# Kernel tuning notes

Hardware: AMD Instinct MI355X
Metric: run time of the kernel (lower is better)

## Reference

```python
import jax, jax.numpy as jnp
import numpy as np

BLOCK = 64       # _aether_cfg['block_size']
JL_DIM = 32      # epsilon_jl_bridge d_out
EPS_GOV = 0.5    # fixed governor eps (governor.target)
ROPE_BASE = 10000.0
RMS_EPS = 1e-6


def _normalize(x, axis=-1):
    n = jnp.sqrt(jnp.sum(x * x, axis=axis, keepdims=True))
    return x / jnp.maximum(n, 1e-12)


def _rms_norm(x):
    return x * jax.lax.rsqrt(jnp.mean(x * x, axis=-1, keepdims=True) + RMS_EPS)


def _rope(x, cos, sin):
    half = x.shape[-1] // 2
    x1, x2 = x[..., :half], x[..., half:]
    return jnp.concatenate([x1 * cos + x2 * sin, -x1 * sin + x2 * cos], axis=-1)


def setup_inputs() -> dict:
    key = jax.random.key(0)
    ks = jax.random.split(key, 6)
    B, S, Dm, H = 2, 2048, 2048, 16
    sc = 1.0 / np.sqrt(Dm)
    x = jax.random.normal(ks[0], (B, S, Dm), jnp.float32)
    Wq = jax.random.normal(ks[1], (Dm, Dm), jnp.float32) * sc
    Wk = jax.random.normal(ks[2], (Dm, Dm), jnp.float32) * sc
    Wv = jax.random.normal(ks[3], (Dm, Dm), jnp.float32) * sc
    Wo = jax.random.normal(ks[4], (Dm, Dm), jnp.float32) * sc
    q_gain = jnp.ones((H,), jnp.float32)
    return {"x": x, "Wq": Wq, "Wk": Wk, "Wv": Wv, "Wo": Wo, "q_gain": q_gain}


def reference(x, Wq, Wk, Wv, Wo, q_gain):
    B, S, Dm = x.shape
    H = q_gain.shape[0]
    Dh = Dm // H

    # QKV projections (bias-free linear, torch weight layout [out,in])
    q = (x @ Wq.T).reshape(B, S, H, Dh).transpose(0, 2, 1, 3)  # (B,H,S,Dh)
    k = (x @ Wk.T).reshape(B, S, H, Dh).transpose(0, 2, 1, 3)
    v = (x @ Wv.T).reshape(B, S, H, Dh).transpose(0, 2, 1, 3)

    # RoPE tables
    inv_freq = 1.0 / (ROPE_BASE ** (jnp.arange(0, Dh, 2, dtype=jnp.float32) / Dh))
    freqs = jnp.outer(jnp.arange(S, dtype=jnp.float32), inv_freq)  # (S,Dh/2)
    cos = jnp.cos(freqs)[None, None]
    sin = jnp.sin(freqs)[None, None]

    q = _rope(_rms_norm(q), cos, sin) * q_gain[None, :, None, None]
    k = _rope(_rms_norm(k), cos, sin)

    # --- aether sparse SDPA: JL block bounds -> top-k blocks -> gather -> SDPA ---
    N = S // BLOCK  # number of KV blocks (static)
    proj = jax.random.normal(jax.random.key(42), (Dh, JL_DIM), jnp.float32) / np.sqrt(JL_DIM)

    q_proj = _normalize(q.mean(axis=2, keepdims=True) @ proj)          # (B,H,1,JL)
    k_blocks = k.reshape(B, H, N, BLOCK, Dh)
    k_proj = _normalize(k_blocks @ proj)                               # (B,H,N,BLOCK,JL)
    centroids = _normalize(k_proj.mean(axis=3))                        # (B,H,N,JL)
    radii = jnp.clip(
        1.0 - jnp.min(jnp.sum(k_proj * centroids[:, :, :, None, :], axis=-1), axis=-1),
        0.0, 1.0)                                                      # (B,H,N)
    ub = jnp.einsum('bhqj,bhnj->bhqn', q_proj, centroids) + radii[:, :, None, :]
    scores = ub[:, :, 0, :]                                            # (B,H,N)
    # force-include the last two blocks (union in the original code)
    scores = scores.at[:, :, N - 2:].set(jnp.inf)

    n_keep = max(2, int(N * min(1.0, EPS_GOV))) + 2                    # static
    _, top_idx = jax.lax.top_k(scores, n_keep)                         # (B,H,n_keep)
    top_idx = jnp.sort(top_idx, axis=-1)
    idx = (top_idx[..., None] * BLOCK + jnp.arange(BLOCK)).reshape(B, H, -1)  # (B,H,K)

    k_s = jnp.take_along_axis(k, idx[..., None], axis=2)               # (B,H,K,Dh)
    v_s = jnp.take_along_axis(v, idx[..., None], axis=2)

    att = jax.nn.softmax(
        jnp.einsum('bhqd,bhkd->bhqk', q, k_s) / np.sqrt(Dh), axis=-1)  # (B,H,S,K)
    y = jnp.einsum('bhqk,bhkd->bhqd', att, v_s)                        # (B,H,S,Dh)

    y = y.transpose(0, 2, 1, 3).reshape(B, S, Dm)
    return y @ Wo.T
```

## Files before the change

### kernel.cpp

```cpp
#include <hip/hip_runtime.h>
#include <hip/hip_bf16.h>

#define B_ 2
#define S_ 2048
#define DM 2048
#define H_ 16
#define DH 128
#define NBLK 32
#define NKEEP 18
#define BH (B_ * H_)

typedef __attribute__((ext_vector_type(8))) short short8;
typedef __attribute__((ext_vector_type(8))) _Float16 f16x8;
typedef __attribute__((ext_vector_type(4))) _Float16 f16x4;
typedef __attribute__((ext_vector_type(4))) float f32x4;

#define GLOAD16(gp, lp)                                                        \
  __builtin_amdgcn_global_load_lds(                                            \
      (const __attribute__((address_space(1))) unsigned int*)(const void*)(gp),\
      (__attribute__((address_space(3))) unsigned int*)(void*)(lp), 16, 0, 0)

__device__ __forceinline__ unsigned short f32_to_bf16(float f) {
  unsigned u = __float_as_uint(f);
  unsigned r = (u + 0x7fffu + ((u >> 16) & 1u)) >> 16;
  return (unsigned short)r;
}
__device__ __forceinline__ float bf16_to_f32(unsigned short h) {
  return __uint_as_float(((unsigned)h) << 16);
}
__device__ __forceinline__ float fexp2(float x) {
  float r;
  asm("v_exp_f32 %0, %1" : "=v"(r) : "v"(x));
  return r;
}

__device__ __forceinline__ unsigned rotl32(unsigned x, int r) {
  return (x << r) | (x >> (32 - r));
}

__device__ __forceinline__ float erfinv_f32(float x) {
  float w = -log1pf(-x * x);
  float p;
  if (w < 5.0f) {
    w -= 2.5f;
    p = 2.81022636e-08f;
    p = fmaf(p, w, 3.43273939e-07f);
    p = fmaf(p, w, -3.5233877e-06f);
    p = fmaf(p, w, -4.39150654e-06f);
    p = fmaf(p, w, 0.00021858087f);
    p = fmaf(p, w, -0.00125372503f);
    p = fmaf(p, w, -0.00417768164f);
    p = fmaf(p, w, 0.246640727f);
    p = fmaf(p, w, 1.50140941f);
  } else {
    w = sqrtf(w) - 3.0f;
    p = -0.000200214257f;
    p = fmaf(p, w, 0.000100950558f);
    p = fmaf(p, w, 0.00134934322f);
    p = fmaf(p, w, -0.00367342844f);
    p = fmaf(p, w, 0.00573950773f);
    p = fmaf(p, w, -0.0076224613f);
    p = fmaf(p, w, 0.00943887047f);
    p = fmaf(p, w, 1.00167406f);
    p = fmaf(p, w, 2.83297682f);
  }
  return p * x;
}

__device__ __forceinline__ float bits_to_normal(unsigned b) {
  float f = __uint_as_float((b >> 9) | 0x3f800000u) - 1.0f;
  const float lo = -0.9999999403953552f;
  float u = fmaxf(lo, fmaf(f, 2.0f, lo));
  return 1.4142135623730951f * erfinv_f32(u);
}

__global__ void tables_kernel(float* __restrict__ proj,
                              float* __restrict__ cosb,
                              float* __restrict__ sinb) {
  if (blockIdx.x < 16) {
    int i = blockIdx.x * 256 + threadIdx.x;
    unsigned k0 = 0u, k1 = 42u;
    unsigned k2 = 0x1BD11BDAu ^ k0 ^ k1;
    unsigned x0 = 0u, x1 = (unsigned)i;
    x0 += k0; x1 += k1;
#define QR(r) { x0 += x1; x1 = rotl32(x1, r); x1 ^= x0; }
    QR(13) QR(15) QR(26) QR(6)   x0 += k1; x1 += k2 + 1u;
    QR(17) QR(29) QR(16) QR(24)  x0 += k2; x1 += k0 + 2u;
    QR(13) QR(15) QR(26) QR(6)   x0 += k0; x1 += k1 + 3u;
    QR(17) QR(29) QR(16) QR(24)  x0 += k1; x1 += k2 + 4u;
    QR(13) QR(15) QR(26) QR(6)   x0 += k2; x1 += k0 + 5u;
#undef QR
    proj[i] = bits_to_normal(x0 ^ x1) / 5.656854249492381f;
  } else {
    int s = blockIdx.x - 16;
    int j = threadIdx.x;
    if (j < 64) {
      double e = (double)(2 * j) / 128.0;
      double invf = 1.0 / pow(10000.0, e);
      float freq = (float)s * (float)invf;
      cosb[s * 64 + j] = (float)cos((double)freq);
      sinb[s * 64 + j] = (float)sin((double)freq);
    }
  }
}

__global__ __launch_bounds__(256) void split_x3_kernel(const float* __restrict__ in,
                                                       unsigned short* __restrict__ hi,
                                                       unsigned short* __restrict__ lo,
                                                       _Float16* __restrict__ f16,
                                                       int n4) {
  int i = blockIdx.x * blockDim.x + threadIdx.x;
  if (i >= n4) return;
  float4 v = ((const float4*)in)[i];
  ushort4 hv, lv;
  f16x4 fv;
  hv.x = f32_to_bf16(v.x); lv.x = f32_to_bf16(v.x - bf16_to_f32(hv.x)); fv[0] = (_Float16)v.x;
  hv.y = f32_to_bf16(v.y); lv.y = f32_to_bf16(v.y - bf16_to_f32(hv.y)); fv[1] = (_Float16)v.y;
  hv.z = f32_to_bf16(v.z); lv.z = f32_to_bf16(v.z - bf16_to_f32(hv.z)); fv[2] = (_Float16)v.z;
  hv.w = f32_to_bf16(v.w); lv.w = f32_to_bf16(v.w - bf16_to_f32(hv.w)); fv[3] = (_Float16)v.w;
  ((ushort4*)hi)[i] = hv;
  ((ushort4*)lo)[i] = lv;
  ((f16x4*)f16)[i] = fv;
}

__global__ __launch_bounds__(256) void split_w3_kernel(const float* __restrict__ wk,
                                                       const float* __restrict__ wq,
                                                       const float* __restrict__ wv,
                                                       unsigned short* __restrict__ khi,
                                                       unsigned short* __restrict__ klo,
                                                       _Float16* __restrict__ qf,
                                                       _Float16* __restrict__ vf,
                                                       int n4) {
  int i = blockIdx.x * blockDim.x + threadIdx.x;
  if (i >= n4) return;
  {
    float4 v = ((const float4*)wk)[i];
    ushort4 hv, lv;
    hv.x = f32_to_bf16(v.x); lv.x = f32_to_bf16(v.x - bf16_to_f32(hv.x));
    hv.y = f32_to_bf16(v.y); lv.y = f32_to_bf16(v.y - bf16_to_f32(hv.y));
    hv.z = f32_to_bf16(v.z); lv.z = f32_to_bf16(v.z - bf16_to_f32(hv.z));
    hv.w = f32_to_bf16(v.w); lv.w = f32_to_bf16(v.w - bf16_to_f32(hv.w));
    ((ushort4*)khi)[i] = hv;
    ((ushort4*)klo)[i] = lv;
  }
  {
    float4 v = ((const float4*)wq)[i];
    f16x4 fv;
    fv[0] = (_Float16)v.x; fv[1] = (_Float16)v.y;
    fv[2] = (_Float16)v.z; fv[3] = (_Float16)v.w;
    ((f16x4*)qf)[i] = fv;
  }
  {
    float4 v = ((const float4*)wv)[i];
    f16x4 fv;
    fv[0] = (_Float16)v.x; fv[1] = (_Float16)v.y;
    fv[2] = (_Float16)v.z; fv[3] = (_Float16)v.w;
    ((f16x4*)vf)[i] = fv;
  }
}

__global__ __launch_bounds__(256) void split_f16_kernel(const float* __restrict__ in,
                                                        _Float16* __restrict__ f16,
                                                        int n4) {
  int i = blockIdx.x * blockDim.x + threadIdx.x;
  if (i >= n4) return;
  float4 v = ((const float4*)in)[i];
  f16x4 fv;
  fv[0] = (_Float16)v.x; fv[1] = (_Float16)v.y;
  fv[2] = (_Float16)v.z; fv[3] = (_Float16)v.w;
  ((f16x4*)f16)[i] = fv;
}

__global__ __launch_bounds__(512, 2) void mfma_gemm_k_sk(const unsigned short* __restrict__ Ahi,
                                                         const unsigned short* __restrict__ Alo,
                                                         const unsigned short* __restrict__ Whi,
                                                         const unsigned short* __restrict__ Wlo,
                                                         float* __restrict__ kp0,
                                                         float* __restrict__ kp1) {
  __shared__ char smem[131072];
  const int t = threadIdx.x, l = t & 63, w = t >> 6;
  const int lin = blockIdx.z * 128 + blockIdx.y * 8 + blockIdx.x;
  const int swz = (lin & 7) * 32 + (lin >> 3);
  const int kz = swz >> 7;
  const int idx = swz & 127;
  const int n0 = (idx & 7) * 256;
  const int m0 = (idx >> 3) * 256;
  const int kbase = kz * 1024;
  float* C = kz ? kp1 : kp0;
  const int wm = w >> 2, wn = w & 3;
  const int lr = l & 15;
  const int lg8 = (l >> 4) * 8;
  const size_t rstep = (size_t)16 * DM;

  const unsigned short* gAh = Ahi + (size_t)(m0 + w * 32 + lr) * DM + lg8;
  const unsigned short* gAl = Alo + (size_t)(m0 + w * 32 + lr) * DM + lg8;
  const unsigned short* gBh = Whi + (size_t)(n0 + w * 32 + lr) * DM + lg8;
  const unsigned short* gBl = Wlo + (size_t)(n0 + w * 32 + lr) * DM + lg8;

  f32x4 acc[8][4];
#pragma unroll
  for (int i = 0; i < 8; ++i)
#pragma unroll
    for (int j = 0; j < 4; ++j) acc[i][j] = (f32x4){0.f, 0.f, 0.f, 0.f};

  {
    char* base = smem + w * 2048;
    GLOAD16(gAh + kbase, base);
    GLOAD16(gAh + rstep + kbase, base + 1024);
    GLOAD16(gAl + kbase, base + 16384);
    GLOAD16(gAl + rstep + kbase, base + 16384 + 1024);
    GLOAD16(gBh + kbase, base + 32768);
    GLOAD16(gBh + rstep + kbase, base + 32768 + 1024);
    GLOAD16(gBl + kbase, base + 49152);
    GLOAD16(gBl + rstep + kbase, base + 49152 + 1024);
  }
  int cur = 0;

#define KQUAD(q)                                                                        \
  {                                                                                     \
    short8 ah0 = *(const short8*)(buf + (wm * 8 + 2 * (q)) * 1024 + l * 16);            \
    short8 ah1 = *(const short8*)(buf + (wm * 8 + 2 * (q) + 1) * 1024 + l * 16);        \
    short8 al0 = *(const short8*)(buf + 16384 + (wm * 8 + 2 * (q)) * 1024 + l * 16);    \
    short8 al1 = *(const short8*)(buf + 16384 + (wm * 8 + 2 * (q) + 1) * 1024 + l * 16);\
    __builtin_amdgcn_s_setprio(1);                                                      \
    _Pragma("unroll")                                                                   \
    for (int n = 0; n < 4; ++n) {                                                       \
      acc[2 * (q)][n] = __builtin_amdgcn_mfma_f32_16x16x32_bf16(ah0, bh[n], acc[2 * (q)][n], 0, 0, 0); \
      acc[2 * (q)][n] = __builtin_amdgcn_mfma_f32_16x16x32_bf16(ah0, bl[n], acc[2 * (q)][n], 0, 0, 0); \
      acc[2 * (q)][n] = __builtin_amdgcn_mfma_f32_16x16x32_bf16(al0, bh[n], acc[2 * (q)][n], 0, 0, 0); \
    }                                                                                   \
    _Pragma("unroll")                                                                   \
    for (int n = 0; n < 4; ++n) {                                                       \
      acc[2 * (q) + 1][n] = __builtin_amdgcn_mfma_f32_16x16x32_bf16(ah1, bh[n], acc[2 * (q) + 1][n], 0, 0, 0); \
      acc[2 * (q) + 1][n] = __builtin_amdgcn_mfma_f32_16x16x32_bf16(ah1, bl[n], acc[2 * (q) + 1][n], 0, 0, 0); \
      acc[2 * (q) + 1][n] = __builtin_amdgcn_mfma_f32_16x16x32_bf16(al1, bh[n], acc[2 * (q) + 1][n], 0, 0, 0); \
    }                                                                                   \
    __builtin_amdgcn_s_setprio(0);                                                      \
  }

  for (int k0 = kbase; k0 < kbase + 1024; k0 += 32) {
    const bool more = (k0 + 32 < kbase + 1024);
    char* buf = smem + cur * 65536;
    char* nb = smem + (cur ^ 1) * 65536 + w * 2048;
    const int kn = k0 + 32;

    if (more) {
      GLOAD16(gBh + kn, nb + 32768);
      GLOAD16(gBh + rstep + kn, nb + 32768 + 1024);
      asm volatile("s_waitcnt vmcnt(2)" ::: "memory");
    } else {
      asm volatile("s_waitcnt vmcnt(0)" ::: "memory");
    }
    __builtin_amdgcn_s_barrier();

    short8 bh[4], bl[4];
#pragma unroll
    for (int f = 0; f < 4; ++f) {
      bh[f] = *(const short8*)(buf + 32768 + (wn * 4 + f) * 1024 + l * 16);
      bl[f] = *(const short8*)(buf + 49152 + (wn * 4 + f) * 1024 + l * 16);
    }
    KQUAD(0);

    if (more) {
      GLOAD16(gBl + kn, nb + 49152);
      GLOAD16(gBl + rstep + kn, nb + 49152 + 1024);
    }
    KQUAD(1);

    if (more) {
      GLOAD16(gAh + kn, nb);
      GLOAD16(gAh + rstep + kn, nb + 1024);
    }
    KQUAD(2);

    if (more) {
      GLOAD16(gAl + kn, nb + 16384);
      GLOAD16(gAl + rstep + kn, nb + 16384 + 1024);
    }
    KQUAD(3);

    __builtin_amdgcn_s_barrier();
    cur ^= 1;
  }
#undef KQUAD

#pragma unroll
  for (int m = 0; m < 8; ++m) {
    int row0 = m0 + wm * 128 + m * 16 + (l >> 4) * 4;
#pragma unroll
    for (int n = 0; n < 4; ++n) {
      int col = n0 + wn * 64 + n * 16 + (l & 15);
      int h = col >> 7, d = col & 127;
#pragma unroll
      for (int r = 0; r < 4; ++r) {
        int mm = row0 + r;
        int b = mm >> 11, s = mm & (S_ - 1);
        C[(((size_t)(b * H_ + h) * S_) + s) * DH + d] = acc[m][n][r];
      }
    }
  }
}

__global__ __launch_bounds__(512, 2) void mfma_gemm_qv(const _Float16* __restrict__ A,
                                                       const _Float16* __restrict__ W,
                                                       float* __restrict__ Cq,
                                                       _Float16* __restrict__ vt) {
  __shared__ char smem[65536];
  const int t = threadIdx.x, l = t & 63, w = t >> 6;
  const int lin = blockIdx.y * gridDim.x + blockIdx.x;
  const int swz = (lin & 7) * 32 + (lin >> 3);
  const int n0 = (swz & 15) * 256;
  const int m0 = (swz >> 4) * 256;
  const int wm = w >> 2, wn = w & 3;
  const int lr = l & 15;
  const int lg8 = (l >> 4) * 8;
  const size_t rstep = (size_t)16 * DM;

  const _Float16* gA = A + (size_t)(m0 + w * 32 + lr) * DM + lg8;
  const _Float16* gB = W + (size_t)(n0 + w * 32 + lr) * DM + lg8;

  f32x4 acc[8][4];
#pragma unroll
  for (int i = 0; i < 8; ++i)
#pragma unroll
    for (int j = 0; j < 4; ++j) acc[i][j] = (f32x4){0.f, 0.f, 0.f, 0.f};

  {
    char* base = smem + w * 2048;
    GLOAD16(gA, base);
    GLOAD16(gA + rstep, base + 1024);
    GLOAD16(gB, base + 16384);
    GLOAD16(gB + rstep, base + 16384 + 1024);
  }
  int cur = 0;

  for (int k0 = 0; k0 < DM; k0 += 32) {
    const bool more = (k0 + 32 < DM);
    char* buf = smem + cur * 32768;
    char* nb = smem + (cur ^ 1) * 32768 + w * 2048;
    const int kn = k0 + 32;

    if (more) {
      GLOAD16(gA + kn, nb);
      GLOAD16(gA + rstep + kn, nb + 1024);
      asm volatile("s_waitcnt vmcnt(2)" ::: "memory");
    } else {
      asm volatile("s_waitcnt vmcnt(0)" ::: "memory");
    }
    __builtin_amdgcn_s_barrier();

    f16x8 b[4];
#pragma unroll
    for (int j = 0; j < 4; ++j)
      b[j] = *(const f16x8*)(buf + 16384 + (wn * 4 + j) * 1024 + l * 16);
    __builtin_amdgcn_s_setprio(1);
#pragma unroll
    for (int i = 0; i < 4; ++i) {
      f16x8 a = *(const f16x8*)(buf + (wm * 8 + i) * 1024 + l * 16);
#pragma unroll
      for (int j = 0; j < 4; ++j)
        acc[i][j] = __builtin_amdgcn_mfma_f32_16x16x32_f16(a, b[j], acc[i][j], 0, 0, 0);
    }
    __builtin_amdgcn_s_setprio(0);

    if (more) {
      GLOAD16(gB + kn, nb + 16384);
      GLOAD16(gB + rstep + kn, nb + 16384 + 1024);
    }
    __builtin_amdgcn_s_setprio(1);
#pragma unroll
    for (int i = 4; i < 8; ++i) {
      f16x8 a = *(const f16x8*)(buf + (wm * 8 + i) * 1024 + l * 16);
#pragma unroll
      for (int j = 0; j < 4; ++j)
        acc[i][j] = __builtin_amdgcn_mfma_f32_16x16x32_f16(a, b[j], acc[i][j], 0, 0, 0);
    }
    __builtin_amdgcn_s_setprio(0);
    __builtin_amdgcn_s_barrier();

    cur ^= 1;
  }

#pragma unroll
  for (int m = 0; m < 8; ++m) {
    int row0 = m0 + wm * 128 + m * 16 + (l >> 4) * 4;
#pragma unroll
    for (int n = 0; n < 4; ++n) {
      int col = n0 + wn * 64 + n * 16 + (l & 15);
      if (col < DM) {
        int h = col >> 7, d = col & 127;
#pragma unroll
        for (int r = 0; r < 4; ++r) {
          int mm = row0 + r;
          int b2 = mm >> 11, s = mm & (S_ - 1);
          Cq[(((size_t)(b2 * H_ + h) * S_) + s) * DH + d] = acc[m][n][r];
        }
      } else {
        int vcol = col - DM;
        int h = vcol >> 7, d = vcol & 127;
        int b2 = row0 >> 11, s0 = row0 & (S_ - 1);
        f16x4 vv;
        vv[0] = (_Float16)acc[m][n][0];
        vv[1] = (_Float16)acc[m][n][1];
        vv[2] = (_Float16)acc[m][n][2];
        vv[3] = (_Float16)acc[m][n][3];
        *(f16x4*)(vt + (((size_t)(b2 * H_ + h)) * DH + d) * S_ + s0) = vv;
      }
    }
  }
}

template <int MODE>
__global__ __launch_bounds__(256) void mfma_gemm_f16(const _Float16* __restrict__ A,
                                                     const _Float16* __restrict__ W,
                                                     void* __restrict__ Cout) {
  __shared__ char smem[65536];
  const int t = threadIdx.x, l = t & 63, w = t >> 6;
  const int lin = blockIdx.y * gridDim.x + blockIdx.x;
  const int cpx = (gridDim.x * gridDim.y) >> 3;
  const int swz = (lin & 7) * cpx + (lin >> 3);
  const int n0 = (swz % gridDim.x) * 128;
  const int m0 = (swz / gridDim.x) * 128;
  const int wm = w >> 1, wn = w & 1;
  const int lr = l & 15;
  const int lg8 = (l >> 4) * 8;

  auto STAGE = [&](int k0, int c) {
    char* base = smem + c * 32768;
#pragma unroll
    for (int f0 = 0; f0 < 4; ++f0) {
      int f = w * 4 + f0;
      int rb = f >> 1, kh = f & 1;
      GLOAD16(A + (size_t)(m0 + rb * 16 + lr) * DM + k0 + kh * 32 + lg8,
              base + f * 1024);
      GLOAD16(W + (size_t)(n0 + rb * 16 + lr) * DM + k0 + kh * 32 + lg8,
              base + 16384 + f * 1024);
    }
  };

  f32x4 acc[4][4];
#pragma unroll
  for (int i = 0; i < 4; ++i)
#pragma unroll
    for (int j = 0; j < 4; ++j) acc[i][j] = (f32x4){0.f, 0.f, 0.f, 0.f};

  STAGE(0, 0);
  int cur = 0;

  for (int k0 = 0; k0 < DM; k0 += 64) {
    if (k0 + 64 < DM) {
      STAGE(k0 + 64, cur ^ 1);
      asm volatile("s_waitcnt vmcnt(8)" ::: "memory");
    } else {
      asm volatile("s_waitcnt vmcnt(0)" ::: "memory");
    }
    __builtin_amdgcn_s_barrier();

    char* buf = smem + cur * 32768;
    f16x8 a[4][2], b[4][2];
#pragma unroll
    for (int i = 0; i < 4; ++i)
#pragma unroll
      for (int kh = 0; kh < 2; ++kh) {
        a[i][kh] = *(const f16x8*)(buf + ((wm * 4 + i) * 2 + kh) * 1024 + l * 16);
        b[i][kh] = *(const f16x8*)(buf + 16384 + ((wn * 4 + i) * 2 + kh) * 1024 + l * 16);
      }
    __builtin_amdgcn_s_setprio(1);
#pragma unroll
    for (int i = 0; i < 4; ++i)
#pragma unroll
      for (int j = 0; j < 4; ++j) {
        acc[i][j] = __builtin_amdgcn_mfma_f32_16x16x32_f16(a[i][0], b[j][0], acc[i][j], 0, 0, 0);
        acc[i][j] = __builtin_amdgcn_mfma_f32_16x16x32_f16(a[i][1], b[j][1], acc[i][j], 0, 0, 0);
      }
    __builtin_amdgcn_s_setprio(0);
    __builtin_amdgcn_s_barrier();
    cur ^= 1;
  }

#pragma unroll
  for (int i = 0; i < 4; ++i) {
    int row0 = m0 + wm * 64 + i * 16 + (l >> 4) * 4;
#pragma unroll
    for (int j = 0; j < 4; ++j) {
      int col = n0 + wn * 64 + j * 16 + (l & 15);
      if constexpr (MODE == 1) {
        float* C = (float*)Cout;
#pragma unroll
        for (int r = 0; r < 4; ++r)
          C[(size_t)(row0 + r) * DM + col] = acc[i][j][r];
      }
    }
  }
}

__global__ __launch_bounds__(256) void rmsrope_k_kernel(float* __restrict__ k,
                                                        const float* __restrict__ kp1,
                                                        _Float16* __restrict__ kf,
                                                        const float* __restrict__ cosb,
                                                        const float* __restrict__ sinb) {
  int w = threadIdx.x >> 6;
  int lane = threadIdx.x & 63;
  long r = (long)blockIdx.x * 4 + w;
  float* p = k + r * DH;
  const float* p1 = kp1 + r * DH;
  int s = (int)(r & (S_ - 1));
  float x1 = p[lane] + p1[lane];
  float x2 = p[lane + 64] + p1[lane + 64];
  float ss = fmaf(x1, x1, x2 * x2);
#pragma unroll
  for (int off = 32; off; off >>= 1) ss += __shfl_xor(ss, off);
  float rms = rsqrtf(ss * (1.0f / 128.0f) + 1e-6f);
  float n1 = x1 * rms, n2 = x2 * rms;
  float c = cosb[s * 64 + lane], sn = sinb[s * 64 + lane];
  float o1 = fmaf(n1, c, n2 * sn);
  float o2 = fmaf(-n1, sn, n2 * c);
  p[lane] = o1;
  p[lane + 64] = o2;
  kf[r * DH + lane] = (_Float16)o1;
  kf[r * DH + lane + 64] = (_Float16)o2;
}

__global__ __launch_bounds__(256) void rmsrope_q_kernel(const float* __restrict__ q,
                                                        _Float16* __restrict__ qf,
                                                        const float* __restrict__ cosb,
                                                        const float* __restrict__ sinb,
                                                        const float* __restrict__ qg,
                                                        float* __restrict__ qpart) {
  __shared__ float red[4][128];
  const float SC = 0.12751743f;
  const int w = threadIdx.x >> 6;
  const int lane = threadIdx.x & 63;
  const int bh = blockIdx.x >> 4, chunk = blockIdx.x & 15;
  const int h = bh & (H_ - 1);
  const float g = qg[h] * SC;
  float s0 = 0.f, s1 = 0.f;
  long rbase = (long)bh * S_ + chunk * 128 + w * 32;
  for (int i = 0; i < 32; ++i) {
    long r = rbase + i;
    const float* p = q + r * DH;
    int s = (int)(r & (S_ - 1));
    float x1 = p[lane], x2 = p[lane + 64];
    float ss = fmaf(x1, x1, x2 * x2);
#pragma unroll
    for (int off = 32; off; off >>= 1) ss += __shfl_xor(ss, off);
    float rms = rsqrtf(ss * (1.0f / 128.0f) + 1e-6f);
    float n1 = x1 * rms, n2 = x2 * rms;
    float c = cosb[s * 64 + lane], sn = sinb[s * 64 + lane];
    float o1 = fmaf(n1, c, n2 * sn) * g;
    float o2 = fmaf(-n1, sn, n2 * c) * g;
    qf[r * DH + lane] = (_Float16)o1;
    qf[r * DH + lane + 64] = (_Float16)o2;
    s0 += o1;
    s1 += o2;
  }
  red[w][lane] = s0;
  red[w][lane + 64] = s1;
  __syncthreads();
  int t = threadIdx.x;
  if (t < 128)
    qpart[(size_t)blockIdx.x * 128 + t] =
        (red[0][t] + red[1][t]) + (red[2][t] + red[3][t]);
}

__global__ void qproj_kernel(const float* __restrict__ partial,
                             const float* __restrict__ proj,
                             float* __restrict__ qp) {
  __shared__ float meanq[128];
  __shared__ float qps[32];
  __shared__ float nrm;
  const int bh = blockIdx.x, t = threadIdx.x;
  float s = 0.0f;
#pragma unroll
  for (int c = 0; c < 16; ++c) s += partial[((size_t)bh * 16 + c) * 128 + t];
  meanq[t] = s * (1.0f / 2048.0f);
  __syncthreads();
  if (t < 32) {
    float sum = 0.0f;
    for (int d = 0; d < 128; ++d) sum = fmaf(meanq[d], proj[d * 32 + t], sum);
    qps[t] = sum;
  }
  __syncthreads();
  if (t == 0) {
    float sum = 0.0f;
    for (int j = 0; j < 32; ++j) sum += qps[j] * qps[j];
    nrm = 1.0f / fmaxf(sqrtf(sum), 1e-12f);
  }
  __syncthreads();
  if (t < 32) qp[bh * 32 + t] = qps[t] * nrm;
}

__global__ __launch_bounds__(256) void kscore_kernel(const float* __restrict__ k,
                                                     const float* __restrict__ proj,
                                                     const float* __restrict__ qp,
                                                     float* __restrict__ scores) {
  __shared__ float ps[128][32];
  __shared__ float kp[64][33];
  __shared__ float cent[33];
  __shared__ float nrm;
  const int bh = blockIdx.x >> 5, n = blockIdx.x & 31;
  const int t = threadIdx.x;
  for (int i = t; i < 4096; i += 256) ps[i >> 5][i & 31] = proj[i];
  const float* kn = k + ((size_t)bh * S_ + n * 64) * DH;
  __syncthreads();
  {
    int row = t >> 2, j0 = (t & 3) * 8;
    float accv[8];
#pragma unroll
    for (int jj = 0; jj < 8; ++jj) accv[jj] = 0.0f;
#pragma unroll 4
    for (int d = 0; d < 128; ++d) {
      float kv = kn[(size_t)row * DH + d];
#pragma unroll
      for (int jj = 0; jj < 8; ++jj) accv[jj] = fmaf(kv, ps[d][j0 + jj], accv[jj]);
    }
#pragma unroll
    for (int jj = 0; jj < 8; ++jj) kp[row][j0 + jj] = accv[jj];
  }
  __syncthreads();
  if (t < 64) {
    float sum = 0.0f;
    for (int j = 0; j < 32; ++j) sum += kp[t][j] * kp[t][j];
    float scl = 1.0f / fmaxf(sqrtf(sum), 1e-12f);
    for (int j = 0; j < 32; ++j) kp[t][j] *= scl;
  }
  __syncthreads();
  if (t < 32) {
    float sum = 0.0f;
    for (int r2 = 0; r2 < 64; ++r2) sum += kp[r2][t];
    cent[t] = sum * (1.0f / 64.0f);
  }
  __syncthreads();
  if (t == 0) {
    float sum = 0.0f;
    for (int j = 0; j < 32; ++j) sum += cent[j] * cent[j];
    nrm = 1.0f / fmaxf(sqrtf(sum), 1e-12f);
  }
  __syncthreads();
  if (t < 32) cent[t] *= nrm;
  __syncthreads();
  if (t < 64) {
    float dt = 0.0f;
    for (int j = 0; j < 32; ++j) dt = fmaf(kp[t][j], cent[j], dt);
#pragma unroll
    for (int off = 32; off; off >>= 1) dt = fminf(dt, __shfl_xor(dt, off));
    if (t == 0) {
      float radius = fminf(fmaxf(1.0f - dt, 0.0f), 1.0f);
      float dq = 0.0f;
      for (int j = 0; j < 32; ++j) dq = fmaf(qp[bh * 32 + j], cent[j], dq);
      scores[bh * 32 + n] = dq + radius;
    }
  }
}

__global__ void topk_kernel(const float* __restrict__ scores, int* __restrict__ top_idx) {
  if (threadIdx.x != 0) return;
  const int bh = blockIdx.x;
  float sc[NBLK];
  for (int j = 0; j < NBLK; ++j) sc[j] = scores[bh * 32 + j];
  sc[NBLK - 2] = INFINITY;
  sc[NBLK - 1] = INFINITY;
  int chosen[NKEEP];
  bool used[NBLK];
  for (int j = 0; j < NBLK; ++j) used[j] = false;
  for (int kk = 0; kk < NKEEP; ++kk) {
    int best = -1;
    float bv = 0.0f;
    for (int j = 0; j < NBLK; ++j)
      if (!used[j] && (best < 0 || sc[j] > bv)) { bv = sc[j]; best = j; }
    used[best] = true;
    chosen[kk] = best;
  }
  for (int a = 1; a < NKEEP; ++a) {
    int v2 = chosen[a], b2 = a - 1;
    while (b2 >= 0 && chosen[b2] > v2) { chosen[b2 + 1] = chosen[b2]; --b2; }
    chosen[b2 + 1] = v2;
  }
  for (int a = 0; a < NKEEP; ++a) top_idx[bh * NKEEP + a] = chosen[a];
}

__global__ __launch_bounds__(256) void attn_mfma_kernel(const _Float16* __restrict__ qfp,
                                                        const _Float16* __restrict__ kf,
                                                        const _Float16* __restrict__ vt,
                                                        const int* __restrict__ top_idx,
                                                        _Float16* __restrict__ yf) {
  __shared__ char lds[74752];
  const int bh = blockIdx.x >> 5;
  const int qt = blockIdx.x & 31;
  const int t = threadIdx.x, l = t & 63, w = t >> 6;
  const int lr = l & 15, lg = l >> 4;
  const float THR2 = 11.5415603f;

  f16x8 qf[4];
  {
    const _Float16* qbase = qfp + ((size_t)(bh * S_ + qt * 64 + w * 16 + lr)) * DH + lg * 8;
#pragma unroll
    for (int dc = 0; dc < 4; ++dc)
      qf[dc] = *(const f16x8*)(qbase + dc * 32);
  }

  float m_[4] = {-INFINITY, -INFINITY, -INFINITY, -INFINITY};
  float ls[4] = {0.f, 0.f, 0.f, 0.f};
  f32x4 yacc[8];
#pragma unroll
  for (int dt = 0; dt < 8; ++dt) yacc[dt] = (f32x4){0.f, 0.f, 0.f, 0.f};

  char* Pw = lds + 65536 + w * 2304;

  const _Float16* kb0 = kf + (size_t)bh * S_ * DH;
  const _Float16* vb0 = vt + (size_t)bh * DH * S_;
  const int* idxp = top_idx + bh * NKEEP;

  auto STAGE = [&](int blk, int c) {
    char* base = lds + c * 32768;
#pragma unroll
    for (int f0 = 0; f0 < 4; ++f0) {
      int f = w * 4 + f0;
      int kt = f >> 2, dc = f & 3;
      GLOAD16(kb0 + (size_t)(blk * 64 + kt * 16 + lr) * DH + dc * 32 + lg * 8,
              base + f * 1024);
      int K0 = f >> 3, dt = f & 7;
      GLOAD16(vb0 + (size_t)(dt * 16 + lr) * S_ + blk * 64 + K0 * 32 + lg * 8,
              base + 16384 + f * 1024);
    }
  };

  int cur = 0;
  STAGE(idxp[0], 0);

  for (int it = 0; it < NKEEP; ++it) {
    if (it + 1 < NKEEP) {
      STAGE(idxp[it + 1], cur ^ 1);
      asm volatile("s_waitcnt vmcnt(8)" ::: "memory");
    } else {
      asm volatile("s_waitcnt vmcnt(0)" ::: "memory");
    }
    __builtin_amdgcn_s_barrier();
    char* buf = lds + cur * 32768;

    f32x4 sacc[4];
#pragma unroll
    for (int kt = 0; kt < 4; ++kt) sacc[kt] = (f32x4){0.f, 0.f, 0.f, 0.f};
    __builtin_amdgcn_s_setprio(1);
#pragma unroll
    for (int kt = 0; kt < 4; ++kt)
#pragma unroll
      for (int dc = 0; dc < 4; ++dc) {
        f16x8 kfr = *(const f16x8*)(buf + (kt * 4 + dc) * 1024 + l * 16);
        sacc[kt] = __builtin_amdgcn_mfma_f32_16x16x32_f16(qf[dc], kfr, sacc[kt], 0, 0, 0);
      }
    __builtin_amdgcn_s_setprio(0);

    float lmax[4];
#pragma unroll
    for (int r = 0; r < 4; ++r)
      lmax[r] = fmaxf(fmaxf(sacc[0][r], sacc[1][r]), fmaxf(sacc[2][r], sacc[3][r]));
    bool ok = (lmax[0] <= m_[0] + THR2) && (lmax[1] <= m_[1] + THR2) &&
              (lmax[2] <= m_[2] + THR2) && (lmax[3] <= m_[3] + THR2);
    float p[4][4];
    if (__all(ok)) {
#pragma unroll
      for (int r = 0; r < 4; ++r) {
#pragma unroll
        for (int kt = 0; kt < 4; ++kt) {
          p[kt][r] = fexp2(sacc[kt][r] - m_[r]);
          ls[r] += p[kt][r];
        }
      }
    } else {
#pragma unroll
      for (int r = 0; r < 4; ++r) {
        float mv = lmax[r];
#pragma unroll
        for (int off = 1; off < 16; off <<= 1) mv = fmaxf(mv, __shfl_xor(mv, off));
        float mn = fmaxf(m_[r], mv);
        float corr = fexp2(m_[r] - mn);
        float rs = 0.f;
#pragma unroll
        for (int kt = 0; kt < 4; ++kt) {
          p[kt][r] = fexp2(sacc[kt][r] - mn);
          rs += p[kt][r];
        }
        ls[r] = ls[r] * corr + rs;
        m_[r] = mn;
#pragma unroll
        for (int dt = 0; dt < 8; ++dt) yacc[dt][r] *= corr;
      }
    }

#pragma unroll
    for (int kt = 0; kt < 4; ++kt)
#pragma unroll
      for (int r = 0; r < 4; ++r)
        *(_Float16*)(Pw + (lg * 4 + r) * 144 + (kt * 16 + lr) * 2) = (_Float16)p[kt][r];

    __builtin_amdgcn_s_setprio(1);
#pragma unroll
    for (int K0 = 0; K0 < 2; ++K0) {
      f16x8 pa = *(const f16x8*)(Pw + lr * 144 + K0 * 64 + lg * 16);
#pragma unroll
      for (int dt = 0; dt < 8; ++dt) {
        f16x8 vf = *(const f16x8*)(buf + 16384 + (K0 * 8 + dt) * 1024 + l * 16);
        yacc[dt] = __builtin_amdgcn_mfma_f32_16x16x32_f16(pa, vf, yacc[dt], 0, 0, 0);
      }
    }
    __builtin_amdgcn_s_setprio(0);

    __builtin_amdgcn_s_barrier();
    cur ^= 1;
  }

  const int b = bh >> 4, h = bh & (H_ - 1);
  float inv[4];
#pragma unroll
  for (int r = 0; r < 4; ++r) {
    float s = ls[r];
#pragma unroll
    for (int off = 1; off < 16; off <<= 1) s += __shfl_xor(s, off);
    inv[r] = 1.0f / s;
  }
#pragma unroll
  for (int r = 0; r < 4; ++r) {
    int srow = qt * 64 + w * 16 + lg * 4 + r;
    size_t off0 = ((size_t)b * S_ + srow) * DM + h * DH + lr;
#pragma unroll
    for (int dt = 0; dt < 8; ++dt)
      yf[off0 + dt * 16] = (_Float16)(yacc[dt][r] * inv[r]);
  }
}

extern "C" void kernel_launch(void* const* d_in, const int* in_sizes, int n_in,
                              void* d_out, int out_size, void* d_ws, size_t ws_size,
                              hipStream_t stream) {
  const float* x  = (const float*)d_in[0];
  const float* Wq = (const float*)d_in[1];
  const float* Wk = (const float*)d_in[2];
  const float* Wv = (const float*)d_in[3];
  const float* Wo = (const float*)d_in[4];
  const float* qg = (const float*)d_in[5];
  float* out = (float*)d_out;

  const size_t NE = (size_t)BH * S_ * DH;
  const size_t WE = (size_t)DM * DM;
  char* p = (char*)d_ws;
  float* q_ws = (float*)p; p += NE * 4;
  float* k_ws = (float*)p; p += NE * 4;
  unsigned short* xhi = (unsigned short*)p; p += NE * 2;
  unsigned short* xlo = (unsigned short*)p; p += NE * 2;
  _Float16* xf16 = (_Float16*)p; p += NE * 2;
  unsigned short* wkhi = (unsigned short*)p; p += WE * 2;
  unsigned short* wklo = (unsigned short*)p; p += WE * 2;
  _Float16* wqv = (_Float16*)p; p += 2 * WE * 2;
  float* cosb = (float*)p; p += (size_t)S_ * 64 * 4;
  float* sinb = (float*)p; p += (size_t)S_ * 64 * 4;
  float* projb = (float*)p; p += 4096 * 4;
  int* idxb = (int*)p; p += BH * NKEEP * 4;
  float* scores = (float*)p; p += BH * NBLK * 4;
  float* qpbuf = (float*)p; p += BH * 32 * 4;
  float* qpart = cosb;
  float* kpart1 = q_ws;
  _Float16* kf16 = (_Float16*)wkhi;
  _Float16* vt = (_Float16*)xlo;
  _Float16* yf16 = (_Float16*)xhi;
  _Float16* qf16 = xf16;
  _Float16* wo = wqv;
  float* qpart2 = (float*)p; p += (size_t)BH * 16 * 128 * 4;
  qpart = qpart2;

  const int nx4 = (int)(NE / 4);
  const int nw4 = (int)(WE / 4);

  tables_kernel<<<dim3(16 + S_), dim3(256), 0, stream>>>(projb, cosb, sinb);
  split_x3_kernel<<<dim3(nx4 / 256), dim3(256), 0, stream>>>(x, xhi, xlo, xf16, nx4);
  split_w3_kernel<<<dim3(nw4 / 256), dim3(256), 0, stream>>>(Wk, Wq, Wv, wkhi, wklo,
                                                             wqv, wqv + WE, nw4);

  mfma_gemm_k_sk<<<dim3(8, 16, 2), dim3(512), 0, stream>>>(xhi, xlo, wkhi, wklo,
                                                           k_ws, kpart1);

  rmsrope_k_kernel<<<dim3((BH * S_) / 4), dim3(256), 0, stream>>>(k_ws, kpart1, kf16, cosb, sinb);

  mfma_gemm_qv<<<dim3(16, 16), dim3(512), 0, stream>>>(xf16, wqv, q_ws, vt);

  rmsrope_q_kernel<<<dim3(BH * 16), dim3(256), 0, stream>>>(q_ws, qf16, cosb, sinb, qg, qpart);

  qproj_kernel<<<dim3(BH), dim3(128), 0, stream>>>(qpart, projb, qpbuf);
  kscore_kernel<<<dim3(BH * NBLK), dim3(256), 0, stream>>>(k_ws, projb, qpbuf, scores);
  topk_kernel<<<dim3(BH), dim3(64), 0, stream>>>(scores, idxb);

  attn_mfma_kernel<<<dim3(BH * 32), dim3(256), 0, stream>>>(qf16, kf16, vt, idxb, yf16);

  split_f16_kernel<<<dim3(nw4 / 256), dim3(256), 0, stream>>>(Wo, wo, nw4);
  mfma_gemm_f16<1><<<dim3(16, 32), dim3(256), 0, stream>>>(yf16, wo, out);
}
```

Baseline: 411.1 us.

## Fuse Q RMSNorm, RoPE and mean partials into QV GEMM epilogue

Re-tiles the QV GEMM warp layout so each wave owns a full 128-wide head (4x8 MFMA tiles), which lets the epilogue apply RMSNorm, RoPE, gain and the per-chunk column sums for Q in registers. The fp32 Q intermediate and the separate rmsrope_q kernel go away, removing a large global write and read round trip plus one launch. The trade-off is a heavier epilogue with shuffles and scattered cos/sin loads inside the GEMM. Workspace aliasing changes: qf16 and qpart now live in the q_ws region.

```diff
diff --git a/kernel.cpp b/kernel.cpp
--- a/kernel.cpp
+++ b/kernel.cpp
@@ -303,7 +303,11 @@
 
 __global__ __launch_bounds__(512, 2) void mfma_gemm_qv(const _Float16* __restrict__ A,
                                                        const _Float16* __restrict__ W,
-                                                       float* __restrict__ Cq,
+                                                       const float* __restrict__ cosb,
+                                                       const float* __restrict__ sinb,
+                                                       const float* __restrict__ qg,
+                                                       _Float16* __restrict__ qf,
+                                                       float* __restrict__ qpart,
                                                        _Float16* __restrict__ vt) {
   __shared__ char smem[65536];
   const int t = threadIdx.x, l = t & 63, w = t >> 6;
@@ -311,19 +315,20 @@
   const int swz = (lin & 7) * 32 + (lin >> 3);
   const int n0 = (swz & 15) * 256;
   const int m0 = (swz >> 4) * 256;
-  const int wm = w >> 2, wn = w & 3;
+  const int wm = w >> 1, wn = w & 1;
   const int lr = l & 15;
-  const int lg8 = (l >> 4) * 8;
+  const int lg = l >> 4;
+  const int lg8 = lg * 8;
   const size_t rstep = (size_t)16 * DM;
 
   const _Float16* gA = A + (size_t)(m0 + w * 32 + lr) * DM + lg8;
   const _Float16* gB = W + (size_t)(n0 + w * 32 + lr) * DM + lg8;
 
-  f32x4 acc[8][4];
-#pragma unroll
-  for (int i = 0; i < 8; ++i)
-#pragma unroll
-    for (int j = 0; j < 4; ++j) acc[i][j] = (f32x4){0.f, 0.f, 0.f, 0.f};
+  f32x4 acc[4][8];
+#pragma unroll
+  for (int i = 0; i < 4; ++i)
+#pragma unroll
+    for (int j = 0; j < 8; ++j) acc[i][j] = (f32x4){0.f, 0.f, 0.f, 0.f};
 
   {
     char* base = smem + w * 2048;
@@ -349,17 +354,17 @@
     }
     __builtin_amdgcn_s_barrier();
 
-    f16x8 b[4];
-#pragma unroll
-    for (int j = 0; j < 4; ++j)
-      b[j] = *(const f16x8*)(buf + 16384 + (wn * 4 + j) * 1024 + l * 16);
+    f16x8 a[4];
+#pragma unroll
+    for (int m = 0; m < 4; ++m)
+      a[m] = *(const f16x8*)(buf + (wm * 4 + m) * 1024 + l * 16);
     __builtin_amdgcn_s_setprio(1);
 #pragma unroll
-    for (int i = 0; i < 4; ++i) {
-      f16x8 a = *(const f16x8*)(buf + (wm * 8 + i) * 1024 + l * 16);
-#pragma unroll
-      for (int j = 0; j < 4; ++j)
-        acc[i][j] = __builtin_amdgcn_mfma_f32_16x16x32_f16(a, b[j], acc[i][j], 0, 0, 0);
+    for (int n = 0; n < 4; ++n) {
+      f16x8 b = *(const f16x8*)(buf + 16384 + (wn * 8 + n) * 1024 + l * 16);
+#pragma unroll
+      for (int m = 0; m < 4; ++m)
+        acc[m][n] = __builtin_amdgcn_mfma_f32_16x16x32_f16(a[m], b, acc[m][n], 0, 0, 0);
     }
     __builtin_amdgcn_s_setprio(0);
 
@@ -369,11 +374,11 @@
     }
     __builtin_amdgcn_s_setprio(1);
 #pragma unroll
-    for (int i = 4; i < 8; ++i) {
-      f16x8 a = *(const f16x8*)(buf + (wm * 8 + i) * 1024 + l * 16);
-#pragma unroll
-      for (int j = 0; j < 4; ++j)
-        acc[i][j] = __builtin_amdgcn_mfma_f32_16x16x32_f16(a, b[j], acc[i][j], 0, 0, 0);
+    for (int n = 4; n < 8; ++n) {
+      f16x8 b = *(const f16x8*)(buf + 16384 + (wn * 8 + n) * 1024 + l * 16);
+#pragma unroll
+      for (int m = 0; m < 4; ++m)
+        acc[m][n] = __builtin_amdgcn_mfma_f32_16x16x32_f16(a[m], b, acc[m][n], 0, 0, 0);
     }
     __builtin_amdgcn_s_setprio(0);
     __builtin_amdgcn_s_barrier();
@@ -381,24 +386,60 @@
     cur ^= 1;
   }
 
-#pragma unroll
-  for (int m = 0; m < 8; ++m) {
-    int row0 = m0 + wm * 128 + m * 16 + (l >> 4) * 4;
-#pragma unroll
-    for (int n = 0; n < 4; ++n) {
-      int col = n0 + wn * 64 + n * 16 + (l & 15);
-      if (col < DM) {
-        int h = col >> 7, d = col & 127;
-#pragma unroll
-        for (int r = 0; r < 4; ++r) {
-          int mm = row0 + r;
-          int b2 = mm >> 11, s = mm & (S_ - 1);
-          Cq[(((size_t)(b2 * H_ + h) * S_) + s) * DH + d] = acc[m][n][r];
+  const int b2 = m0 >> 11;
+  const int sbase = (m0 & (S_ - 1)) + wm * 64;
+
+  if (n0 < DM) {
+    const int h = (n0 >> 7) + wn;
+    const float g = qg[h] * 0.12751743f;
+    float csum[8];
+#pragma unroll
+    for (int n = 0; n < 8; ++n) csum[n] = 0.f;
+#pragma unroll
+    for (int m = 0; m < 4; ++m) {
+#pragma unroll
+      for (int r = 0; r < 4; ++r) {
+        int srow = sbase + m * 16 + lg * 4 + r;
+        float ss = 0.f;
+#pragma unroll
+        for (int n = 0; n < 8; ++n) ss = fmaf(acc[m][n][r], acc[m][n][r], ss);
+#pragma unroll
+        for (int off = 1; off < 16; off <<= 1) ss += __shfl_xor(ss, off);
+        float rms = rsqrtf(ss * (1.0f / 128.0f) + 1e-6f);
+        size_t rowoff = ((size_t)(b2 * H_ + h) * S_ + srow) * DH;
+#pragma unroll
+        for (int n = 0; n < 4; ++n) {
+          int j = n * 16 + lr;
+          float c = cosb[srow * 64 + j], sn = sinb[srow * 64 + j];
+          float x1 = acc[m][n][r] * rms, x2 = acc[m][n + 4][r] * rms;
+          float o1 = fmaf(x1, c, x2 * sn) * g;
+          float o2 = fmaf(-x1, sn, x2 * c) * g;
+          qf[rowoff + j] = (_Float16)o1;
+          qf[rowoff + j + 64] = (_Float16)o2;
+          csum[n] += o1;
+          csum[n + 4] += o2;
         }
-      } else {
-        int vcol = col - DM;
-        int h = vcol >> 7, d = vcol & 127;
-        int b2 = row0 >> 11, s0 = row0 & (S_ - 1);
+      }
+    }
+#pragma unroll
+    for (int n = 0; n < 8; ++n) {
+      csum[n] += __shfl_xor(csum[n], 16);
+      csum[n] += __shfl_xor(csum[n], 32);
+    }
+    if (lg == 0) {
+      int chunk = sbase >> 6;
+      size_t base = (((size_t)(b2 * H_ + h) * 32) + chunk) * 128;
+#pragma unroll
+      for (int n = 0; n < 8; ++n) qpart[base + n * 16 + lr] = csum[n];
+    }
+  } else {
+    const int h = ((n0 - DM) >> 7) + wn;
+#pragma unroll
+    for (int m = 0; m < 4; ++m) {
+      int s0 = sbase + m * 16 + lg * 4;
+#pragma unroll
+      for (int n = 0; n < 8; ++n) {
+        int d = n * 16 + lr;
         f16x4 vv;
         vv[0] = (_Float16)acc[m][n][0];
         vv[1] = (_Float16)acc[m][n][1];
@@ -521,48 +562,6 @@
   kf[r * DH + lane + 64] = (_Float16)o2;
 }
 
-__global__ __launch_bounds__(256) void rmsrope_q_kernel(const float* __restrict__ q,
-                                                        _Float16* __restrict__ qf,
-                                                        const float* __restrict__ cosb,
-                                                        const float* __restrict__ sinb,
-                                                        const float* __restrict__ qg,
-                                                        float* __restrict__ qpart) {
-  __shared__ float red[4][128];
-  const float SC = 0.12751743f;
-  const int w = threadIdx.x >> 6;
-  const int lane = threadIdx.x & 63;
-  const int bh = blockIdx.x >> 4, chunk = blockIdx.x & 15;
-  const int h = bh & (H_ - 1);
-  const float g = qg[h] * SC;
-  float s0 = 0.f, s1 = 0.f;
-  long rbase = (long)bh * S_ + chunk * 128 + w * 32;
-  for (int i = 0; i < 32; ++i) {
-    long r = rbase + i;
-    const float* p = q + r * DH;
-    int s = (int)(r & (S_ - 1));
-    float x1 = p[lane], x2 = p[lane + 64];
-    float ss = fmaf(x1, x1, x2 * x2);
-#pragma unroll
-    for (int off = 32; off; off >>= 1) ss += __shfl_xor(ss, off);
-    float rms = rsqrtf(ss * (1.0f / 128.0f) + 1e-6f);
-    float n1 = x1 * rms, n2 = x2 * rms;
-    float c = cosb[s * 64 + lane], sn = sinb[s * 64 + lane];
-    float o1 = fmaf(n1, c, n2 * sn) * g;
-    float o2 = fmaf(-n1, sn, n2 * c) * g;
-    qf[r * DH + lane] = (_Float16)o1;
-    qf[r * DH + lane + 64] = (_Float16)o2;
-    s0 += o1;
-    s1 += o2;
-  }
-  red[w][lane] = s0;
-  red[w][lane + 64] = s1;
-  __syncthreads();
-  int t = threadIdx.x;
-  if (t < 128)
-    qpart[(size_t)blockIdx.x * 128 + t] =
-        (red[0][t] + red[1][t]) + (red[2][t] + red[3][t]);
-}
-
 __global__ void qproj_kernel(const float* __restrict__ partial,
                              const float* __restrict__ proj,
                              float* __restrict__ qp) {
@@ -572,7 +571,7 @@
   const int bh = blockIdx.x, t = threadIdx.x;
   float s = 0.0f;
 #pragma unroll
-  for (int c = 0; c < 16; ++c) s += partial[((size_t)bh * 16 + c) * 128 + t];
+  for (int c = 0; c < 32; ++c) s += partial[((size_t)bh * 32 + c) * 128 + t];
   meanq[t] = s * (1.0f / 2048.0f);
   __syncthreads();
   if (t < 32) {
@@ -857,15 +856,13 @@
   int* idxb = (int*)p; p += BH * NKEEP * 4;
   float* scores = (float*)p; p += BH * NBLK * 4;
   float* qpbuf = (float*)p; p += BH * 32 * 4;
-  float* qpart = cosb;
   float* kpart1 = q_ws;
+  _Float16* qf16 = (_Float16*)q_ws;
+  float* qpart = (float*)((char*)q_ws + NE * 2);
   _Float16* kf16 = (_Float16*)wkhi;
   _Float16* vt = (_Float16*)xlo;
   _Float16* yf16 = (_Float16*)xhi;
-  _Float16* qf16 = xf16;
   _Float16* wo = wqv;
-  float* qpart2 = (float*)p; p += (size_t)BH * 16 * 128 * 4;
-  qpart = qpart2;
 
   const int nx4 = (int)(NE / 4);
   const int nw4 = (int)(WE / 4);
@@ -880,9 +877,8 @@
 
   rmsrope_k_kernel<<<dim3((BH * S_) / 4), dim3(256), 0, stream>>>(k_ws, kpart1, kf16, cosb, sinb);
 
-  mfma_gemm_qv<<<dim3(16, 16), dim3(512), 0, stream>>>(xf16, wqv, q_ws, vt);
-
-  rmsrope_q_kernel<<<dim3(BH * 16), dim3(256), 0, stream>>>(q_ws, qf16, cosb, sinb, qg, qpart);
+  mfma_gemm_qv<<<dim3(16, 16), dim3(512), 0, stream>>>(xf16, wqv, cosb, sinb, qg,
+                                                       qf16, qpart, vt);
 
   qproj_kernel<<<dim3(BH), dim3(128), 0, stream>>>(qpart, projb, qpbuf);
   kscore_kernel<<<dim3(BH * NBLK), dim3(256), 0, stream>>>(k_ws, projb, qpbuf, scores);
```

After: 397.4 us. -3.3%, faster.
